# Optimization experiments

Hardware: AMD Instinct MI355X
Metric: run time of the kernel (lower is better)

The kernel has to match this reference:

```python
import jax, jax.numpy as jnp
import numpy as np

D_IN = 1024
D_OUT = 1024
SEQ = 4096


def setup_inputs() -> dict:
    key = jax.random.key(0)
    k0, k1, k2, k3 = jax.random.split(key, 4)
    inputs = jax.random.normal(k0, (SEQ, D_IN), dtype=jnp.float32)
    # original uses torch.rand (uniform [0,1)) for weights
    W_q = jax.random.uniform(k1, (D_IN, D_OUT), dtype=jnp.float32)
    W_k = jax.random.uniform(k2, (D_IN, D_OUT), dtype=jnp.float32)
    W_v = jax.random.uniform(k3, (D_IN, D_OUT), dtype=jnp.float32)
    return {"inputs": inputs, "W_q": W_q, "W_k": W_k, "W_v": W_v}


def reference(inputs, W_q, W_k, W_v):
    queries = inputs @ W_q            # [S, d_out]
    keys = inputs @ W_k               # [S, d_out]
    values = inputs @ W_v             # [S, d_out]
    d_k = keys.shape[-1]
    scale = 1.0 / jnp.sqrt(jnp.asarray(d_k, dtype=queries.dtype))
    attn_scores = queries @ keys.T    # [S, S]
    attn_weights = jax.nn.softmax(attn_scores * scale, axis=-1)
    context_vectors = attn_weights @ values  # [S, d_out]
    return context_vectors
```

## Files before the change

kernel.cpp:

```cpp
#include <hip/hip_runtime.h>

typedef unsigned short u16;
typedef __attribute__((ext_vector_type(8))) short bf16x8;
typedef __attribute__((ext_vector_type(4))) float f32x4;

#define SEQ 4096
#define DIM 1024

__device__ __forceinline__ u16 f2bf(float f) {
  unsigned u = __float_as_uint(f);
  return (u16)((u + 0x7fffu + ((u >> 16) & 1u)) >> 16);
}
__device__ __forceinline__ float bf2f(u16 h) {
  return __uint_as_float(((unsigned)h) << 16);
}

__device__ __forceinline__ void gload_lds16(const void* g, void* l) {
  __builtin_amdgcn_global_load_lds(
      (const __attribute__((address_space(1))) void*)g,
      (__attribute__((address_space(3))) void*)l, 16, 0, 0);
}

__device__ __forceinline__ size_t pkoff(int row, int col, int kd) {
  int tile = (row >> 7) * (kd >> 5) + (col >> 5);
  int r7 = row & 127, c5 = col & 31;
  int slot = ((r7 >> 4) << 6) | ((c5 >> 3) << 4) | (r7 & 15);
  return (size_t)tile * 4096 + (size_t)(slot * 8 + (c5 & 7));
}

__device__ __forceinline__ void stage_tile_pk(const u16* __restrict__ g,
                                              u16* lds, int tid) {
  const int w = tid >> 6;
  gload_lds16(g + (size_t)tid * 8, lds + (size_t)(w * 64) * 8);
  gload_lds16(g + (size_t)(256 + tid) * 8, lds + (size_t)(256 + w * 64) * 8);
}

__device__ __forceinline__ void gemm3_db(
    const u16* A0, const u16* A1, const u16* B0, const u16* B1,
    int nkb, u16* lds, f32x4 (&acc)[4][4]) {
  const int tid = threadIdx.x;
  const int w = tid >> 6, l = tid & 63;
  const int wm = w >> 1, wn = w & 1;

#pragma unroll
  for (int mi = 0; mi < 4; ++mi)
#pragma unroll
    for (int ni = 0; ni < 4; ++ni)
      acc[mi][ni] = (f32x4){0.f, 0.f, 0.f, 0.f};

  const int ao = wm * 2048 + l * 8;
  const int bo = wn * 2048 + l * 8;

  stage_tile_pk(A0, lds, tid);
  stage_tile_pk(B0, lds + 4096, tid);
  stage_tile_pk(A1, lds + 8192, tid);
  stage_tile_pk(B1, lds + 12288, tid);

  for (int kb = 0; kb < nkb; ++kb) {
    __syncthreads();
    if (kb + 1 < nkb) {
      u16* nb = lds + ((kb + 1) & 1) * 16384;
      const size_t off = (size_t)(kb + 1) * 4096;
      stage_tile_pk(A0 + off, nb, tid);
      stage_tile_pk(B0 + off, nb + 4096, tid);
      stage_tile_pk(A1 + off, nb + 8192, tid);
      stage_tile_pk(B1 + off, nb + 12288, tid);
    }
    const u16* cb = lds + (kb & 1) * 16384;
    const u16* lA0 = cb;
    const u16* lB0 = cb + 4096;
    const u16* lA1 = cb + 8192;
    const u16* lB1 = cb + 12288;

    bf16x8 a0[4], b0[4];
#pragma unroll
    for (int i = 0; i < 4; ++i) {
      a0[i] = *(const bf16x8*)(lA0 + ao + i * 512);
      b0[i] = *(const bf16x8*)(lB0 + bo + i * 512);
    }
#pragma unroll
    for (int mi = 0; mi < 4; ++mi)
#pragma unroll
      for (int ni = 0; ni < 4; ++ni)
        acc[mi][ni] = __builtin_amdgcn_mfma_f32_16x16x32_bf16(
            a0[mi], b0[ni], acc[mi][ni], 0, 0, 0);
    bf16x8 b1[4];
#pragma unroll
    for (int i = 0; i < 4; ++i) b1[i] = *(const bf16x8*)(lB1 + bo + i * 512);
#pragma unroll
    for (int mi = 0; mi < 4; ++mi)
#pragma unroll
      for (int ni = 0; ni < 4; ++ni)
        acc[mi][ni] = __builtin_amdgcn_mfma_f32_16x16x32_bf16(
            a0[mi], b1[ni], acc[mi][ni], 0, 0, 0);
    bf16x8 a1[4];
#pragma unroll
    for (int i = 0; i < 4; ++i) a1[i] = *(const bf16x8*)(lA1 + ao + i * 512);
#pragma unroll
    for (int mi = 0; mi < 4; ++mi)
#pragma unroll
      for (int ni = 0; ni < 4; ++ni)
        acc[mi][ni] = __builtin_amdgcn_mfma_f32_16x16x32_bf16(
            a1[mi], b0[ni], acc[mi][ni], 0, 0, 0);
  }
  __syncthreads();
}

__device__ __forceinline__ void gemm1_db(
    const u16* A, const u16* B, int nkb, u16* lds, f32x4 (&acc)[4][4]) {
  const int tid = threadIdx.x;
  const int w = tid >> 6, l = tid & 63;
  const int wm = w >> 1, wn = w & 1;

#pragma unroll
  for (int mi = 0; mi < 4; ++mi)
#pragma unroll
    for (int ni = 0; ni < 4; ++ni)
      acc[mi][ni] = (f32x4){0.f, 0.f, 0.f, 0.f};

  const int ao = wm * 2048 + l * 8;
  const int bo = wn * 2048 + l * 8;
  const int nit = nkb >> 1;

  stage_tile_pk(A, lds, tid);
  stage_tile_pk(A + 4096, lds + 4096, tid);
  stage_tile_pk(B, lds + 8192, tid);
  stage_tile_pk(B + 4096, lds + 12288, tid);

  for (int it = 0; it < nit; ++it) {
    __syncthreads();
    if (it + 1 < nit) {
      u16* nb = lds + ((it + 1) & 1) * 16384;
      const size_t off = (size_t)(it + 1) * 8192;
      stage_tile_pk(A + off, nb, tid);
      stage_tile_pk(A + off + 4096, nb + 4096, tid);
      stage_tile_pk(B + off, nb + 8192, tid);
      stage_tile_pk(B + off + 4096, nb + 12288, tid);
    }
    const u16* cb = lds + (it & 1) * 16384;
#pragma unroll
    for (int ht = 0; ht < 2; ++ht) {
      bf16x8 av[4], bv[4];
#pragma unroll
      for (int i = 0; i < 4; ++i) {
        av[i] = *(const bf16x8*)(cb + ht * 4096 + ao + i * 512);
        bv[i] = *(const bf16x8*)(cb + 8192 + ht * 4096 + bo + i * 512);
      }
#pragma unroll
      for (int mi = 0; mi < 4; ++mi)
#pragma unroll
        for (int ni = 0; ni < 4; ++ni)
          acc[mi][ni] = __builtin_amdgcn_mfma_f32_16x16x32_bf16(
              av[mi], bv[ni], acc[mi][ni], 0, 0, 0);
    }
  }
  __syncthreads();
}

#define EPILOGUE_IDX                                          \
  const int tid = threadIdx.x, w = tid >> 6, l = tid & 63;    \
  const int wm = w >> 1, wn = w & 1, lr = l & 15, q = l >> 4; \
  (void)tid;


__global__ __launch_bounds__(256) void prep_kernel(
    const float* __restrict__ X,
    const float* __restrict__ W0, const float* __restrict__ W1, const float* __restrict__ W2,
    u16* __restrict__ Xh, u16* __restrict__ Xl,
    u16* __restrict__ H0, u16* __restrict__ L0,
    u16* __restrict__ H1, u16* __restrict__ L1,
    u16* __restrict__ H2) {
  const int z = blockIdx.z;
  const int tx = threadIdx.x, ty = threadIdx.y;
  if (z == 0) {
    int idx = (blockIdx.y * 32 + blockIdx.x) * 256 + ty * 32 + tx;
    int row = idx >> 6;
    int c0 = (idx & 63) * 16;
    u16 h[16], lo[16];
#pragma unroll
    for (int j = 0; j < 4; ++j) {
      float4 x = *(const float4*)(X + (size_t)row * DIM + c0 + j * 4);
      float v;
      v = x.x; h[j*4+0] = f2bf(v); lo[j*4+0] = f2bf(v - bf2f(h[j*4+0]));
      v = x.y; h[j*4+1] = f2bf(v); lo[j*4+1] = f2bf(v - bf2f(h[j*4+1]));
      v = x.z; h[j*4+2] = f2bf(v); lo[j*4+2] = f2bf(v - bf2f(h[j*4+2]));
      v = x.w; h[j*4+3] = f2bf(v); lo[j*4+3] = f2bf(v - bf2f(h[j*4+3]));
    }
    size_t o0 = pkoff(row, c0, DIM);
    size_t o1 = pkoff(row, c0 + 8, DIM);
    *(bf16x8*)(Xh + o0) = *(bf16x8*)(h);
    *(bf16x8*)(Xl + o0) = *(bf16x8*)(lo);
    *(bf16x8*)(Xh + o1) = *(bf16x8*)(h + 8);
    *(bf16x8*)(Xl + o1) = *(bf16x8*)(lo + 8);
    return;
  }
  __shared__ float t[32][33];
  const float* W = (z == 1) ? W0 : (z == 2) ? W1 : W2;
  u16* H = (z == 1) ? H0 : (z == 2) ? H1 : H2;
  u16* L = (z == 1) ? L0 : (z == 2) ? L1 : nullptr;
  const int i0 = blockIdx.y * 32, o0 = blockIdx.x * 32;
#pragma unroll
  for (int m = 0; m < 4; ++m)
    t[ty + 8 * m][tx] = W[(size_t)(i0 + ty + 8 * m) * DIM + o0 + tx];
  __syncthreads();
#pragma unroll
  for (int m = 0; m < 4; ++m) {
    float v = t[tx][ty + 8 * m];
    u16 h = f2bf(v);
    size_t o = pkoff(o0 + ty + 8 * m, i0 + tx, DIM);
    H[o] = h;
    if (L) L[o] = f2bf(v - bf2f(h));
  }
}

__global__ __launch_bounds__(256) void qkv_kernel(
    const u16* __restrict__ Xh, const u16* __restrict__ Xl,
    const u16* __restrict__ Wh0, const u16* __restrict__ Wl0,
    const u16* __restrict__ Wh1, const u16* __restrict__ Wl1,
    const u16* __restrict__ Wh2,
    u16* __restrict__ Qh, u16* __restrict__ Ql,
    u16* __restrict__ Kh, u16* __restrict__ Kl,
    u16* __restrict__ VT) {
  __shared__ __align__(16) u16 lds[2 * 4 * 4096];
  const int z = blockIdx.z;
  f32x4 acc[4][4];
  if (z < 2) {
    const u16* Wh = z ? Wh1 : Wh0;
    const u16* Wl = z ? Wl1 : Wl0;
    const int row0 = blockIdx.y * 128, col0 = blockIdx.x * 128;
    gemm3_db(Xh + (size_t)row0 * DIM, Xl + (size_t)row0 * DIM,
             Wh + (size_t)col0 * DIM, Wl + (size_t)col0 * DIM,
             DIM / 32, lds, acc);
    EPILOGUE_IDX
    u16* H = z ? Kh : Qh;
    u16* L = z ? Kl : Ql;
#pragma unroll
    for (int mi = 0; mi < 4; ++mi)
#pragma unroll
      for (int ni = 0; ni < 4; ++ni)
#pragma unroll
        for (int r = 0; r < 4; ++r) {
          int row = row0 + wm * 64 + mi * 16 + q * 4 + r;
          int col = col0 + wn * 64 + ni * 16 + lr;
          float v = acc[mi][ni][r];
          u16 h = f2bf(v);
          size_t o = pkoff(row, col, DIM);
          H[o] = h;
          L[o] = f2bf(v - bf2f(h));
        }
  } else {
    const int row0 = blockIdx.x * 128;
    const int col0 = blockIdx.y * 128;
    gemm1_db(Wh2 + (size_t)row0 * DIM, Xh + (size_t)col0 * DIM,
             DIM / 32, lds, acc);
    EPILOGUE_IDX
#pragma unroll
    for (int mi = 0; mi < 4; ++mi)
#pragma unroll
      for (int ni = 0; ni < 4; ++ni)
#pragma unroll
        for (int r = 0; r < 4; ++r) {
          int row = row0 + wm * 64 + mi * 16 + q * 4 + r;
          int col = col0 + wn * 64 + ni * 16 + lr;
          VT[pkoff(row, col, SEQ)] = f2bf(acc[mi][ni][r]);
        }
  }
}

__global__ __launch_bounds__(256) void s_kernel(
    const u16* __restrict__ Qh, const u16* __restrict__ Ql,
    const u16* __restrict__ Kh, const u16* __restrict__ Kl,
    float* __restrict__ S) {
  __shared__ __align__(16) u16 lds[2 * 4 * 4096];
  const int row0 = blockIdx.y * 128, col0 = blockIdx.x * 128;
  f32x4 acc[4][4];
  gemm3_db(Qh + (size_t)row0 * DIM, Ql + (size_t)row0 * DIM,
           Kh + (size_t)col0 * DIM, Kl + (size_t)col0 * DIM,
           DIM / 32, lds, acc);
  EPILOGUE_IDX
  const float scale = 0.03125f;
#pragma unroll
  for (int mi = 0; mi < 4; ++mi)
#pragma unroll
    for (int ni = 0; ni < 4; ++ni)
#pragma unroll
      for (int r = 0; r < 4; ++r) {
        int row = row0 + wm * 64 + mi * 16 + q * 4 + r;
        int col = col0 + wn * 64 + ni * 16 + lr;
        S[(size_t)row * SEQ + col] = acc[mi][ni][r] * scale;
      }
}

__global__ __launch_bounds__(256) void softmax_kernel(const float* __restrict__ S,
                                                      u16* __restrict__ P) {
  const int row = blockIdx.x;
  const float* s = S + (size_t)row * SEQ;
  const int tid = threadIdx.x;
  const int c0 = tid * 16;
  float v[16];
  float mx = -3.4e38f;
#pragma unroll
  for (int j = 0; j < 4; ++j) {
    float4 x = *(const float4*)(s + c0 + j * 4);
    v[j * 4 + 0] = x.x; v[j * 4 + 1] = x.y; v[j * 4 + 2] = x.z; v[j * 4 + 3] = x.w;
    mx = fmaxf(mx, fmaxf(fmaxf(x.x, x.y), fmaxf(x.z, x.w)));
  }
#pragma unroll
  for (int off = 32; off; off >>= 1) mx = fmaxf(mx, __shfl_xor(mx, off));
  __shared__ float red[8];
  const int w = tid >> 6, l = tid & 63;
  if (l == 0) red[w] = mx;
  __syncthreads();
  mx = fmaxf(fmaxf(red[0], red[1]), fmaxf(red[2], red[3]));
  float sum = 0.f;
#pragma unroll
  for (int i = 0; i < 16; ++i) {
    v[i] = __expf(v[i] - mx);
    sum += v[i];
  }
#pragma unroll
  for (int off = 32; off; off >>= 1) sum += __shfl_xor(sum, off);
  if (l == 0) red[4 + w] = sum;
  __syncthreads();
  sum = red[4] + red[5] + red[6] + red[7];
  const float inv = 1.f / sum;
  u16 p[16];
#pragma unroll
  for (int i = 0; i < 16; ++i) p[i] = f2bf(v[i] * inv);
  *(bf16x8*)(P + pkoff(row, c0, SEQ)) = *(bf16x8*)(p);
  *(bf16x8*)(P + pkoff(row, c0 + 8, SEQ)) = *(bf16x8*)(p + 8);
}

__global__ __launch_bounds__(256) void o_kernel(const u16* __restrict__ P,
                                                const u16* __restrict__ VT,
                                                float* __restrict__ Opart) {
  __shared__ __align__(16) u16 lds[2 * 4 * 4096];
  const int z = blockIdx.z;
  const int row0 = blockIdx.y * 128, col0 = blockIdx.x * 128;
  const u16* A = P + (size_t)row0 * SEQ + (size_t)z * 32 * 4096;
  const u16* B = VT + (size_t)col0 * SEQ + (size_t)z * 32 * 4096;
  f32x4 acc[4][4];
  gemm1_db(A, B, 32, lds, acc);
  EPILOGUE_IDX
  float* O = Opart + (size_t)z * SEQ * DIM;
#pragma unroll
  for (int mi = 0; mi < 4; ++mi)
#pragma unroll
    for (int ni = 0; ni < 4; ++ni)
#pragma unroll
      for (int r = 0; r < 4; ++r) {
        int row = row0 + wm * 64 + mi * 16 + q * 4 + r;
        int col = col0 + wn * 64 + ni * 16 + lr;
        O[(size_t)row * DIM + col] = acc[mi][ni][r];
      }
}

__global__ __launch_bounds__(256) void o_reduce_kernel(const float* __restrict__ Op,
                                                       float* __restrict__ O) {
  const size_t N = (size_t)SEQ * DIM;
  size_t i = ((size_t)blockIdx.x * 256 + threadIdx.x) * 4;
  float4 a = *(const float4*)(Op + i);
  float4 b = *(const float4*)(Op + N + i);
  float4 c = *(const float4*)(Op + 2 * N + i);
  float4 d = *(const float4*)(Op + 3 * N + i);
  float4 rr;
  rr.x = (a.x + b.x) + (c.x + d.x);
  rr.y = (a.y + b.y) + (c.y + d.y);
  rr.z = (a.z + b.z) + (c.z + d.z);
  rr.w = (a.w + b.w) + (c.w + d.w);
  *(float4*)(O + i) = rr;
}

extern "C" void kernel_launch(void* const* d_in, const int* in_sizes, int n_in,
                              void* d_out, int out_size, void* d_ws, size_t ws_size,
                              hipStream_t stream) {
  const float* X = (const float*)d_in[0];
  const float* Wq = (const float*)d_in[1];
  const float* Wk = (const float*)d_in[2];
  const float* Wv = (const float*)d_in[3];

  const size_t MB = 1024 * 1024;
  char* w = (char*)d_ws;
  u16* Xh = (u16*)(w + 0 * MB);
  u16* Xl = (u16*)(w + 8 * MB);
  u16* WqhT = (u16*)(w + 16 * MB);
  u16* WqlT = (u16*)(w + 18 * MB);
  u16* WkhT = (u16*)(w + 20 * MB);
  u16* WklT = (u16*)(w + 22 * MB);
  u16* WvhT = (u16*)(w + 24 * MB);
  u16* Qh = (u16*)(w + 26 * MB);
  u16* Ql = (u16*)(w + 34 * MB);
  u16* Kh = (u16*)(w + 42 * MB);
  u16* Kl = (u16*)(w + 50 * MB);
  u16* VT = (u16*)(w + 58 * MB);
  float* S = (float*)(w + 66 * MB);
  u16* P = (u16*)(w + 26 * MB);
  float* Opart = (float*)(w + 66 * MB);

  prep_kernel<<<dim3(32, 32, 4), dim3(32, 8), 0, stream>>>(
      X, Wq, Wk, Wv, Xh, Xl, WqhT, WqlT, WkhT, WklT, WvhT);
  qkv_kernel<<<dim3(DIM / 128, SEQ / 128, 3), 256, 0, stream>>>(
      Xh, Xl, WqhT, WqlT, WkhT, WklT, WvhT, Qh, Ql, Kh, Kl, VT);
  s_kernel<<<dim3(SEQ / 128, SEQ / 128), 256, 0, stream>>>(Qh, Ql, Kh, Kl, S);
  softmax_kernel<<<SEQ, 256, 0, stream>>>(S, P);
  o_kernel<<<dim3(DIM / 128, SEQ / 128, 4), 256, 0, stream>>>(P, VT, Opart);
  o_reduce_kernel<<<(SEQ * DIM) / (256 * 4), 256, 0, stream>>>(Opart, (float*)d_out);
}
```

Measured before the change: 317.9 us.

## Load A fragments directly from global into registers, halve LDS; split-K 4→2

The GEMM helpers stop staging the A operand through LDS. Each wave now loads its A fragments straight from global memory into registers, with even/odd register double buffering, while only B goes through LDS. This halves shared-memory use per block, which may raise occupancy and cuts LDS traffic. The o_kernel split-K factor also drops from 4 to 2, which removes half the partial-sum traffic in the reduce at the cost of fewer blocks. The risks are global-load latency sitting directly in the MFMA path, more register pressure, and lower parallelism in the O GEMM.

```diff
diff --git a/kernel.cpp b/kernel.cpp
--- a/kernel.cpp
+++ b/kernel.cpp
@@ -35,7 +35,15 @@
   gload_lds16(g + (size_t)(256 + tid) * 8, lds + (size_t)(256 + w * 64) * 8);
 }
 
-__device__ __forceinline__ void gemm3_db(
+__device__ __forceinline__ void load_afrags(const u16* __restrict__ A,
+                                            size_t off, int wm, int l,
+                                            bf16x8 (&a)[4]) {
+#pragma unroll
+  for (int mi = 0; mi < 4; ++mi)
+    a[mi] = *(const bf16x8*)(A + off + (size_t)((wm * 4 + mi) * 512 + l * 8));
+}
+
+__device__ __forceinline__ void gemm3_ad(
     const u16* A0, const u16* A1, const u16* B0, const u16* B1,
     int nkb, u16* lds, f32x4 (&acc)[4][4]) {
   const int tid = threadIdx.x;
@@ -48,65 +56,62 @@
     for (int ni = 0; ni < 4; ++ni)
       acc[mi][ni] = (f32x4){0.f, 0.f, 0.f, 0.f};
 
-  const int ao = wm * 2048 + l * 8;
   const int bo = wn * 2048 + l * 8;
-
-  stage_tile_pk(A0, lds, tid);
-  stage_tile_pk(B0, lds + 4096, tid);
-  stage_tile_pk(A1, lds + 8192, tid);
-  stage_tile_pk(B1, lds + 12288, tid);
-
-  for (int kb = 0; kb < nkb; ++kb) {
+  bf16x8 a0e[4], a1e[4], a0o[4], a1o[4];
+
+  load_afrags(A0, 0, wm, l, a0e);
+  load_afrags(A1, 0, wm, l, a1e);
+  stage_tile_pk(B0, lds, tid);
+  stage_tile_pk(B1, lds + 4096, tid);
+
+#define G3_COMPUTE(buf, a0c, a1c)                                          \
+  {                                                                        \
+    const u16* lB0 = lds + (buf) * 8192;                                   \
+    const u16* lB1 = lds + (buf) * 8192 + 4096;                            \
+    bf16x8 b0[4], b1[4];                                                   \
+    _Pragma("unroll") for (int i = 0; i < 4; ++i)                          \
+        b0[i] = *(const bf16x8*)(lB0 + bo + i * 512);                      \
+    _Pragma("unroll") for (int mi = 0; mi < 4; ++mi)                       \
+        _Pragma("unroll") for (int ni = 0; ni < 4; ++ni)                   \
+            acc[mi][ni] = __builtin_amdgcn_mfma_f32_16x16x32_bf16(         \
+                a0c[mi], b0[ni], acc[mi][ni], 0, 0, 0);                    \
+    _Pragma("unroll") for (int i = 0; i < 4; ++i)                          \
+        b1[i] = *(const bf16x8*)(lB1 + bo + i * 512);                      \
+    _Pragma("unroll") for (int mi = 0; mi < 4; ++mi)                       \
+        _Pragma("unroll") for (int ni = 0; ni < 4; ++ni)                   \
+            acc[mi][ni] = __builtin_amdgcn_mfma_f32_16x16x32_bf16(         \
+                a0c[mi], b1[ni], acc[mi][ni], 0, 0, 0);                    \
+    _Pragma("unroll") for (int mi = 0; mi < 4; ++mi)                       \
+        _Pragma("unroll") for (int ni = 0; ni < 4; ++ni)                   \
+            acc[mi][ni] = __builtin_amdgcn_mfma_f32_16x16x32_bf16(         \
+                a1c[mi], b0[ni], acc[mi][ni], 0, 0, 0);                    \
+  }
+
+  for (int kb = 0; kb < nkb; kb += 2) {
     __syncthreads();
-    if (kb + 1 < nkb) {
-      u16* nb = lds + ((kb + 1) & 1) * 16384;
+    {
       const size_t off = (size_t)(kb + 1) * 4096;
-      stage_tile_pk(A0 + off, nb, tid);
-      stage_tile_pk(B0 + off, nb + 4096, tid);
-      stage_tile_pk(A1 + off, nb + 8192, tid);
-      stage_tile_pk(B1 + off, nb + 12288, tid);
+      stage_tile_pk(B0 + off, lds + 8192, tid);
+      stage_tile_pk(B1 + off, lds + 12288, tid);
+      load_afrags(A0, off, wm, l, a0o);
+      load_afrags(A1, off, wm, l, a1o);
     }
-    const u16* cb = lds + (kb & 1) * 16384;
-    const u16* lA0 = cb;
-    const u16* lB0 = cb + 4096;
-    const u16* lA1 = cb + 8192;
-    const u16* lB1 = cb + 12288;
-
-    bf16x8 a0[4], b0[4];
-#pragma unroll
-    for (int i = 0; i < 4; ++i) {
-      a0[i] = *(const bf16x8*)(lA0 + ao + i * 512);
-      b0[i] = *(const bf16x8*)(lB0 + bo + i * 512);
+    G3_COMPUTE(0, a0e, a1e)
+    __syncthreads();
+    if (kb + 2 < nkb) {
+      const size_t off = (size_t)(kb + 2) * 4096;
+      stage_tile_pk(B0 + off, lds, tid);
+      stage_tile_pk(B1 + off, lds + 4096, tid);
+      load_afrags(A0, off, wm, l, a0e);
+      load_afrags(A1, off, wm, l, a1e);
     }
-#pragma unroll
-    for (int mi = 0; mi < 4; ++mi)
-#pragma unroll
-      for (int ni = 0; ni < 4; ++ni)
-        acc[mi][ni] = __builtin_amdgcn_mfma_f32_16x16x32_bf16(
-            a0[mi], b0[ni], acc[mi][ni], 0, 0, 0);
-    bf16x8 b1[4];
-#pragma unroll
-    for (int i = 0; i < 4; ++i) b1[i] = *(const bf16x8*)(lB1 + bo + i * 512);
-#pragma unroll
-    for (int mi = 0; mi < 4; ++mi)
-#pragma unroll
-      for (int ni = 0; ni < 4; ++ni)
-        acc[mi][ni] = __builtin_amdgcn_mfma_f32_16x16x32_bf16(
-            a0[mi], b1[ni], acc[mi][ni], 0, 0, 0);
-    bf16x8 a1[4];
-#pragma unroll
-    for (int i = 0; i < 4; ++i) a1[i] = *(const bf16x8*)(lA1 + ao + i * 512);
-#pragma unroll
-    for (int mi = 0; mi < 4; ++mi)
-#pragma unroll
-      for (int ni = 0; ni < 4; ++ni)
-        acc[mi][ni] = __builtin_amdgcn_mfma_f32_16x16x32_bf16(
-            a1[mi], b0[ni], acc[mi][ni], 0, 0, 0);
+    G3_COMPUTE(1, a0o, a1o)
   }
   __syncthreads();
-}
-
-__device__ __forceinline__ void gemm1_db(
+#undef G3_COMPUTE
+}
+
+__device__ __forceinline__ void gemm1_ad(
     const u16* A, const u16* B, int nkb, u16* lds, f32x4 (&acc)[4][4]) {
   const int tid = threadIdx.x;
   const int w = tid >> 6, l = tid & 63;
@@ -118,43 +123,49 @@
     for (int ni = 0; ni < 4; ++ni)
       acc[mi][ni] = (f32x4){0.f, 0.f, 0.f, 0.f};
 
-  const int ao = wm * 2048 + l * 8;
   const int bo = wn * 2048 + l * 8;
+  bf16x8 ae[8], ao[8];
   const int nit = nkb >> 1;
 
-  stage_tile_pk(A, lds, tid);
-  stage_tile_pk(A + 4096, lds + 4096, tid);
-  stage_tile_pk(B, lds + 8192, tid);
-  stage_tile_pk(B + 4096, lds + 12288, tid);
-
-  for (int it = 0; it < nit; ++it) {
+  load_afrags(A, 0, wm, l, *(bf16x8(*)[4])(ae));
+  load_afrags(A, 4096, wm, l, *(bf16x8(*)[4])(ae + 4));
+  stage_tile_pk(B, lds, tid);
+  stage_tile_pk(B + 4096, lds + 4096, tid);
+
+#define G1_COMPUTE(buf, ac)                                                \
+  _Pragma("unroll") for (int ht = 0; ht < 2; ++ht) {                       \
+    const u16* lB = lds + (buf) * 8192 + ht * 4096;                        \
+    bf16x8 bv[4];                                                          \
+    _Pragma("unroll") for (int i = 0; i < 4; ++i)                          \
+        bv[i] = *(const bf16x8*)(lB + bo + i * 512);                       \
+    _Pragma("unroll") for (int mi = 0; mi < 4; ++mi)                       \
+        _Pragma("unroll") for (int ni = 0; ni < 4; ++ni)                   \
+            acc[mi][ni] = __builtin_amdgcn_mfma_f32_16x16x32_bf16(         \
+                ac[ht * 4 + mi], bv[ni], acc[mi][ni], 0, 0, 0);            \
+  }
+
+  for (int it = 0; it < nit; it += 2) {
     __syncthreads();
-    if (it + 1 < nit) {
-      u16* nb = lds + ((it + 1) & 1) * 16384;
+    {
       const size_t off = (size_t)(it + 1) * 8192;
-      stage_tile_pk(A + off, nb, tid);
-      stage_tile_pk(A + off + 4096, nb + 4096, tid);
-      stage_tile_pk(B + off, nb + 8192, tid);
-      stage_tile_pk(B + off + 4096, nb + 12288, tid);
+      stage_tile_pk(B + off, lds + 8192, tid);
+      stage_tile_pk(B + off + 4096, lds + 12288, tid);
+      load_afrags(A, off, wm, l, *(bf16x8(*)[4])(ao));
+      load_afrags(A, off + 4096, wm, l, *(bf16x8(*)[4])(ao + 4));
     }
-    const u16* cb = lds + (it & 1) * 16384;
-#pragma unroll
-    for (int ht = 0; ht < 2; ++ht) {
-      bf16x8 av[4], bv[4];
-#pragma unroll
-      for (int i = 0; i < 4; ++i) {
-        av[i] = *(const bf16x8*)(cb + ht * 4096 + ao + i * 512);
-        bv[i] = *(const bf16x8*)(cb + 8192 + ht * 4096 + bo + i * 512);
-      }
-#pragma unroll
-      for (int mi = 0; mi < 4; ++mi)
-#pragma unroll
-        for (int ni = 0; ni < 4; ++ni)
-          acc[mi][ni] = __builtin_amdgcn_mfma_f32_16x16x32_bf16(
-              av[mi], bv[ni], acc[mi][ni], 0, 0, 0);
+    G1_COMPUTE(0, ae)
+    __syncthreads();
+    if (it + 2 < nit) {
+      const size_t off = (size_t)(it + 2) * 8192;
+      stage_tile_pk(B + off, lds, tid);
+      stage_tile_pk(B + off + 4096, lds + 4096, tid);
+      load_afrags(A, off, wm, l, *(bf16x8(*)[4])(ae));
+      load_afrags(A, off + 4096, wm, l, *(bf16x8(*)[4])(ae + 4));
     }
+    G1_COMPUTE(1, ao)
   }
   __syncthreads();
+#undef G1_COMPUTE
 }
 
 #define EPILOGUE_IDX                                          \
@@ -221,14 +232,14 @@
     u16* __restrict__ Qh, u16* __restrict__ Ql,
     u16* __restrict__ Kh, u16* __restrict__ Kl,
     u16* __restrict__ VT) {
-  __shared__ __align__(16) u16 lds[2 * 4 * 4096];
+  __shared__ __align__(16) u16 lds[2 * 2 * 4096];
   const int z = blockIdx.z;
   f32x4 acc[4][4];
   if (z < 2) {
     const u16* Wh = z ? Wh1 : Wh0;
     const u16* Wl = z ? Wl1 : Wl0;
     const int row0 = blockIdx.y * 128, col0 = blockIdx.x * 128;
-    gemm3_db(Xh + (size_t)row0 * DIM, Xl + (size_t)row0 * DIM,
+    gemm3_ad(Xh + (size_t)row0 * DIM, Xl + (size_t)row0 * DIM,
              Wh + (size_t)col0 * DIM, Wl + (size_t)col0 * DIM,
              DIM / 32, lds, acc);
     EPILOGUE_IDX
@@ -251,7 +262,7 @@
   } else {
     const int row0 = blockIdx.x * 128;
     const int col0 = blockIdx.y * 128;
-    gemm1_db(Wh2 + (size_t)row0 * DIM, Xh + (size_t)col0 * DIM,
+    gemm1_ad(Wh2 + (size_t)row0 * DIM, Xh + (size_t)col0 * DIM,
              DIM / 32, lds, acc);
     EPILOGUE_IDX
 #pragma unroll
@@ -271,10 +282,10 @@
     const u16* __restrict__ Qh, const u16* __restrict__ Ql,
     const u16* __restrict__ Kh, const u16* __restrict__ Kl,
     float* __restrict__ S) {
-  __shared__ __align__(16) u16 lds[2 * 4 * 4096];
+  __shared__ __align__(16) u16 lds[2 * 2 * 4096];
   const int row0 = blockIdx.y * 128, col0 = blockIdx.x * 128;
   f32x4 acc[4][4];
-  gemm3_db(Qh + (size_t)row0 * DIM, Ql + (size_t)row0 * DIM,
+  gemm3_ad(Qh + (size_t)row0 * DIM, Ql + (size_t)row0 * DIM,
            Kh + (size_t)col0 * DIM, Kl + (size_t)col0 * DIM,
            DIM / 32, lds, acc);
   EPILOGUE_IDX
@@ -334,13 +345,13 @@
 __global__ __launch_bounds__(256) void o_kernel(const u16* __restrict__ P,
                                                 const u16* __restrict__ VT,
                                                 float* __restrict__ Opart) {
-  __shared__ __align__(16) u16 lds[2 * 4 * 4096];
+  __shared__ __align__(16) u16 lds[2 * 2 * 4096];
   const int z = blockIdx.z;
   const int row0 = blockIdx.y * 128, col0 = blockIdx.x * 128;
-  const u16* A = P + (size_t)row0 * SEQ + (size_t)z * 32 * 4096;
-  const u16* B = VT + (size_t)col0 * SEQ + (size_t)z * 32 * 4096;
+  const u16* A = P + (size_t)row0 * SEQ + (size_t)z * 64 * 4096;
+  const u16* B = VT + (size_t)col0 * SEQ + (size_t)z * 64 * 4096;
   f32x4 acc[4][4];
-  gemm1_db(A, B, 32, lds, acc);
+  gemm1_ad(A, B, 64, lds, acc);
   EPILOGUE_IDX
   float* O = Opart + (size_t)z * SEQ * DIM;
 #pragma unroll
@@ -361,13 +372,11 @@
   size_t i = ((size_t)blockIdx.x * 256 + threadIdx.x) * 4;
   float4 a = *(const float4*)(Op + i);
   float4 b = *(const float4*)(Op + N + i);
-  float4 c = *(const float4*)(Op + 2 * N + i);
-  float4 d = *(const float4*)(Op + 3 * N + i);
   float4 rr;
-  rr.x = (a.x + b.x) + (c.x + d.x);
-  rr.y = (a.y + b.y) + (c.y + d.y);
-  rr.z = (a.z + b.z) + (c.z + d.z);
-  rr.w = (a.w + b.w) + (c.w + d.w);
+  rr.x = a.x + b.x;
+  rr.y = a.y + b.y;
+  rr.z = a.z + b.z;
+  rr.w = a.w + b.w;
   *(float4*)(O + i) = rr;
 }
 
@@ -403,6 +412,6 @@
       Xh, Xl, WqhT, WqlT, WkhT, WklT, WvhT, Qh, Ql, Kh, Kl, VT);
   s_kernel<<<dim3(SEQ / 128, SEQ / 128), 256, 0, stream>>>(Qh, Ql, Kh, Kl, S);
   softmax_kernel<<<SEQ, 256, 0, stream>>>(S, P);
-  o_kernel<<<dim3(DIM / 128, SEQ / 128, 4), 256, 0, stream>>>(P, VT, Opart);
+  o_kernel<<<dim3(DIM / 128, SEQ / 128, 2), 256, 0, stream>>>(P, VT, Opart);
   o_reduce_kernel<<<(SEQ * DIM) / (256 * 4), 256, 0, stream>>>(Opart, (float*)d_out);
 }
```

New measurement: 344.3 us. +8.3%, slower.
